# Optimization experiments

Hardware: AMD Instinct MI355X
Metric: run time of the kernel (lower is better)

## Reference

```python
import jax, jax.numpy as jnp
import numpy as np

N = 131072
MUL = 32

# e3nn normalization (irrep_normalization='component', path_normalization='element'):
# alpha_path = w3j_norm * sqrt(ir_out.dim / sum_{paths into same i_out} mul1*mul2)
# 0e output: paths (0e,0e)->0e and (1o,1o)->0e -> fan = 2*32*32 = 2048
# 1o output: paths (0e,1o)->1o and (1o,0e)->1o -> fan = 2048
# 1e output: path  (1o,1o)->1e               -> fan = 1024
_A000 = 1.0 / np.sqrt(2048.0)                    # w3j(0,0,0)=1,        sqrt(1/2048)
_A011 = (1.0 / np.sqrt(3.0)) * np.sqrt(3.0 / 2048.0)   # = 1/sqrt(2048)
_A101 = _A011
_A110 = (1.0 / np.sqrt(3.0)) * np.sqrt(1.0 / 2048.0)
_A111 = (1.0 / np.sqrt(6.0)) * np.sqrt(3.0 / 1024.0)   # = 1/sqrt(2048)


def setup_inputs() -> dict:
    key = jax.random.key(0)
    ks = jax.random.split(key, 7)
    return {
        "x1": jax.random.normal(ks[0], (N, 4 * MUL), dtype=jnp.float32),
        "x2": jax.random.normal(ks[1], (N, 4 * MUL), dtype=jnp.float32),
        "w000": jax.random.normal(ks[2], (MUL, MUL, MUL), dtype=jnp.float32),
        "w011": jax.random.normal(ks[3], (MUL, MUL, MUL), dtype=jnp.float32),
        "w101": jax.random.normal(ks[4], (MUL, MUL, MUL), dtype=jnp.float32),
        "w110": jax.random.normal(ks[5], (MUL, MUL, MUL), dtype=jnp.float32),
        "w111": jax.random.normal(ks[6], (MUL, MUL, MUL), dtype=jnp.float32),
    }


def _uvw(a, b, w):
    # scalar-channel path: out_zw = sum_uv a_zu b_zv w_uvw
    return jnp.einsum('zu,zv,uvw->zw', a, b, w, optimize=True)


def _tp(x1, x2, w000, w011, w101, w110, w111):
    n = x1.shape[0]
    x1s = x1[:, :MUL]                       # [z,u]    0e
    x1v = x1[:, MUL:].reshape(n, MUL, 3)    # [z,u,3]  1o
    x2s = x2[:, :MUL]
    x2v = x2[:, MUL:].reshape(n, MUL, 3)

    # (0e,0e)->0e and (1o,1o)->0e  (w3j(1,1,0) = delta_ij/sqrt(3), folded into alpha)
    p000 = _uvw(x1s, x2s, w000)                                  # [z,w]
    p110 = jnp.einsum('zui,zvi,uvw->zw', x1v, x2v, w110, optimize=True)
    out0 = _A000 * p000 + _A110 * p110                           # [z,w]

    # (0e,1o)->1o and (1o,0e)->1o  (w3j(0,1,1) = delta/sqrt(3), folded into alpha)
    p011 = jnp.einsum('zu,zvj,uvw->zwj', x1s, x2v, w011, optimize=True)
    p101 = jnp.einsum('zui,zv,uvw->zwi', x1v, x2s, w101, optimize=True)
    out1 = _A011 * p011 + _A101 * p101                           # [z,w,3]

    # (1o,1o)->1e via levi-civita (w3j(1,1,1) = eps/sqrt(6), folded into alpha)
    # out_zwk = sum_ij eps_ijk * uvw-contraction; expand cross product per component
    comps = []
    for (i, j) in ((1, 2), (2, 0), (0, 1)):
        comps.append(_uvw(x1v[:, :, i], x2v[:, :, j], w111)
                     - _uvw(x1v[:, :, j], x2v[:, :, i], w111))
    out2 = _A111 * jnp.stack(comps, axis=-1)                     # [z,w,3]

    return jnp.concatenate(
        [out0, out1.reshape(n, -1), out2.reshape(n, -1)], axis=-1)  # [z,224]


def reference(x1, x2, w000, w011, w101, w110, w111):
    return _tp(x1, x2, w000, w011, w101, w110, w111)
```

## Files before the change

### kernel.cpp

```cpp
#include <hip/hip_runtime.h>


typedef _Float16 f16;
typedef f16 f16x8 __attribute__((ext_vector_type(8)));
typedef float f32x4 __attribute__((ext_vector_type(4)));

#define MFMA16(a, b, c) __builtin_amdgcn_mfma_f32_16x16x32_f16(a, b, c, 0, 0, 0)

#define SC_COMMON 0.022097086912079608f
#define SC_110    0.012757759118834242f

__global__ void prep_w(const float* __restrict__ w000, const float* __restrict__ w011,
                       const float* __restrict__ w101, const float* __restrict__ w110,
                       const float* __restrict__ w111, f16* __restrict__ wsW)
{
    int flat = blockIdx.x * 256 + threadIdx.x;
    if (flat >= 5 * 32768) return;
    int c = flat >> 15;
    int r = flat & 32767;
    int j    = r & 7;
    int lane = (r >> 3) & 63;
    int half = (r >> 9) & 1;
    int u    = r >> 10;
    int n = lane & 15, q = lane >> 4;
    int v = q * 8 + j;
    int w = n + 16 * half;
    const float* src; float sc;
    switch (c) {
        case 0: src = w000; sc = SC_COMMON; break;
        case 1: src = w110; sc = SC_110;    break;
        case 2: src = w011; sc = SC_COMMON; break;
        case 3: src = w101; sc = SC_COMMON; break;
        default: src = w111; sc = SC_COMMON; break;
    }
    wsW[flat] = (f16)(sc * src[u * 1024 + v * 32 + w]);
}


template <int A>
__device__ __forceinline__ f16x8 load_group(const float* __restrict__ x1row, int u0)
{
    f16x8 g;
    if (A == 0) {
#pragma unroll
        for (int j = 0; j < 8; ++j) g[j] = (f16)x1row[u0 + j];
    } else {
#pragma unroll
        for (int j = 0; j < 8; ++j) g[j] = (f16)x1row[32 + 3 * (u0 + j) + (A - 1)];
    }
    return g;
}

template <int MODE, int P, int Q>
__device__ __forceinline__ void gemm_half(f32x4 (&acc)[2][2],
                                          const f16* __restrict__ ldsW,
                                          const f16* __restrict__ ldsX2,
                                          const float* __restrict__ x1blk,
                                          int waveRow, int lane, int u0base)
{
    const int m = lane & 15, qd = lane >> 4;

    f16x8 f2a[2], f2b[2], f2c[2];
#pragma unroll
    for (int s = 0; s < 2; ++s) {
        const f16* base = ldsX2 + (waveRow + s * 16 + m) * 128 + qd * 8;
        if (MODE == 0) {
            f2a[s] = *(const f16x8*)(base + Q * 32);
        } else if (MODE == 1) {
            f2a[s] = *(const f16x8*)(base + 1 * 32);
            f2b[s] = *(const f16x8*)(base + 2 * 32);
            f2c[s] = *(const f16x8*)(base + 3 * 32);
        } else {
            f2a[s] = *(const f16x8*)(base + Q * 32);
            f2b[s] = *(const f16x8*)(base + P * 32);
        }
    }

    const float* x1row[2];
#pragma unroll
    for (int s = 0; s < 2; ++s)
        x1row[s] = x1blk + (size_t)(waveRow + s * 16 + m) * 128;

#pragma unroll
    for (int ug = 0; ug < 2; ++ug) {
        const int u0 = u0base + ug * 8;
        f16x8 g1[2], g2[2], g3[2];
#pragma unroll
        for (int s = 0; s < 2; ++s) {
            if (MODE == 0) {
                g1[s] = load_group<P>(x1row[s], u0);
            } else if (MODE == 1) {
                g1[s] = load_group<1>(x1row[s], u0);
                g2[s] = load_group<2>(x1row[s], u0);
                g3[s] = load_group<3>(x1row[s], u0);
            } else {
                g1[s] = load_group<P>(x1row[s], u0);
                g2[s] = load_group<Q>(x1row[s], u0);
            }
        }
#pragma unroll
        for (int uu = 0; uu < 8; ++uu) {
            const int ul = (u0base + ug * 8 + uu) - u0base + (u0base ? 0 : 0);
            const int ulocal = ug * 8 + uu;
            (void)ul;
            f16x8 a[2];
#pragma unroll
            for (int s = 0; s < 2; ++s) {
                if (MODE == 0) {
                    a[s] = g1[s][uu] * f2a[s];
                } else if (MODE == 1) {
                    a[s] = g1[s][uu] * f2a[s] + g2[s][uu] * f2b[s] + g3[s][uu] * f2c[s];
                } else {
                    a[s] = g1[s][uu] * f2a[s] - g2[s][uu] * f2b[s];
                }
            }
#pragma unroll
            for (int half = 0; half < 2; ++half) {
                f16x8 b = *(const f16x8*)(ldsW + ((ulocal * 2 + half) * 64 + lane) * 8);
#pragma unroll
                for (int s = 0; s < 2; ++s)
                    acc[s][half] = MFMA16(a[s], b, acc[s][half]);
            }
        }
    }
}

__device__ __forceinline__ void stage_w(f16* __restrict__ ldsW,
                                        const f16* __restrict__ src, int tid)
{
#pragma unroll
    for (int it = 0; it < 8; ++it) {
        int o = it * 2048 + tid * 8;
        *(f16x8*)(ldsW + o) = *(const f16x8*)(src + o);
    }
}

__global__ __launch_bounds__(256, 2)
void tp_main(const float* __restrict__ x1, const float* __restrict__ x2,
             const f16* __restrict__ wsW, float* __restrict__ out)
{
    __shared__ __align__(16) f16 ldsW[16384];
    __shared__ __align__(16) f16 ldsX2[16384];

    const int tid = threadIdx.x;
    const int lane = tid & 63;
    const int wv = tid >> 6;
    const int waveRow = wv * 32;

    const float* x1blk = x1 + (size_t)blockIdx.x * 128 * 128;
    const float* x2blk = x2 + (size_t)blockIdx.x * 128 * 128;

#pragma unroll
    for (int it = 0; it < 16; ++it) {
        int idx4 = it * 256 + tid;
        float4 val = ((const float4*)x2blk)[idx4];
        float vv[4] = {val.x, val.y, val.z, val.w};
        int flat = idx4 * 4;
        int row = flat >> 7, col = flat & 127;
#pragma unroll
        for (int e = 0; e < 4; ++e) {
            int cc = col + e;
            int arr, ii;
            if (cc < 32) { arr = 0; ii = cc; }
            else { int c2 = cc - 32; arr = 1 + (c2 % 3); ii = c2 / 3; }
            ldsX2[row * 128 + arr * 32 + ii] = (f16)vv[e];
        }
    }

    const int m = lane & 15, qd = lane >> 4;
    const int rowb = blockIdx.x * 128 + waveRow + qd * 4;

    {
        f32x4 acc[2][2] = {};
        for (int c = 0; c < 2; ++c)
            for (int h = 0; h < 2; ++h) {
                __syncthreads();
                stage_w(ldsW, wsW + c * 32768 + h * 16384, tid);
                __syncthreads();
                if (c == 0) gemm_half<0, 0, 0>(acc, ldsW, ldsX2, x1blk, waveRow, lane, h * 16);
                else        gemm_half<1, 0, 0>(acc, ldsW, ldsX2, x1blk, waveRow, lane, h * 16);
            }
#pragma unroll
        for (int s = 0; s < 2; ++s)
#pragma unroll
            for (int half = 0; half < 2; ++half)
#pragma unroll
                for (int r = 0; r < 4; ++r) {
                    int z = rowb + s * 16 + r;
                    out[(size_t)z * 224 + half * 16 + m] = acc[s][half][r];
                }
    }

    {
        f32x4 acc[3][2][2] = {};
        for (int h = 0; h < 2; ++h) {
            __syncthreads();
            stage_w(ldsW, wsW + 2 * 32768 + h * 16384, tid);
            __syncthreads();
            gemm_half<0, 0, 1>(acc[0], ldsW, ldsX2, x1blk, waveRow, lane, h * 16);
            gemm_half<0, 0, 2>(acc[1], ldsW, ldsX2, x1blk, waveRow, lane, h * 16);
            gemm_half<0, 0, 3>(acc[2], ldsW, ldsX2, x1blk, waveRow, lane, h * 16);
        }
        for (int h = 0; h < 2; ++h) {
            __syncthreads();
            stage_w(ldsW, wsW + 3 * 32768 + h * 16384, tid);
            __syncthreads();
            gemm_half<0, 1, 0>(acc[0], ldsW, ldsX2, x1blk, waveRow, lane, h * 16);
            gemm_half<0, 2, 0>(acc[1], ldsW, ldsX2, x1blk, waveRow, lane, h * 16);
            gemm_half<0, 3, 0>(acc[2], ldsW, ldsX2, x1blk, waveRow, lane, h * 16);
        }
#pragma unroll
        for (int s = 0; s < 2; ++s)
#pragma unroll
            for (int half = 0; half < 2; ++half)
#pragma unroll
                for (int r = 0; r < 4; ++r) {
                    int z = rowb + s * 16 + r;
                    int wcol = half * 16 + m;
                    size_t base = (size_t)z * 224 + 32 + 3 * wcol;
                    out[base + 0] = acc[0][s][half][r];
                    out[base + 1] = acc[1][s][half][r];
                    out[base + 2] = acc[2][s][half][r];
                }
    }

    {
        f32x4 acc[3][2][2] = {};
        for (int h = 0; h < 2; ++h) {
            __syncthreads();
            stage_w(ldsW, wsW + 4 * 32768 + h * 16384, tid);
            __syncthreads();
            gemm_half<2, 2, 3>(acc[0], ldsW, ldsX2, x1blk, waveRow, lane, h * 16);
            gemm_half<2, 3, 1>(acc[1], ldsW, ldsX2, x1blk, waveRow, lane, h * 16);
            gemm_half<2, 1, 2>(acc[2], ldsW, ldsX2, x1blk, waveRow, lane, h * 16);
        }
#pragma unroll
        for (int s = 0; s < 2; ++s)
#pragma unroll
            for (int half = 0; half < 2; ++half)
#pragma unroll
                for (int r = 0; r < 4; ++r) {
                    int z = rowb + s * 16 + r;
                    int wcol = half * 16 + m;
                    size_t base = (size_t)z * 224 + 128 + 3 * wcol;
                    out[base + 0] = acc[0][s][half][r];
                    out[base + 1] = acc[1][s][half][r];
                    out[base + 2] = acc[2][s][half][r];
                }
    }
}

extern "C" void kernel_launch(void* const* d_in, const int* in_sizes, int n_in,
                              void* d_out, int out_size, void* d_ws, size_t ws_size,
                              hipStream_t stream)
{
    const float* x1   = (const float*)d_in[0];
    const float* x2   = (const float*)d_in[1];
    const float* w000 = (const float*)d_in[2];
    const float* w011 = (const float*)d_in[3];
    const float* w101 = (const float*)d_in[4];
    const float* w110 = (const float*)d_in[5];
    const float* w111 = (const float*)d_in[6];
    float* out = (float*)d_out;
    f16* wsW = (f16*)d_ws;

    hipLaunchKernelGGL(prep_w, dim3(640), dim3(256), 0, stream,
                       w000, w011, w101, w110, w111, wsW);

    int n = in_sizes[0] / 128;
    hipLaunchKernelGGL(tp_main, dim3(n / 128), dim3(256), 0, stream,
                       x1, x2, wsW, out);
}
```

Measured before the change: 345.6 us.

## Switch to 32x32x16 MFMA with register-resident x1/x2 fragments and async LDS weight staging

Replaces the 16x16x32 MFMA tiling with 32x32x16 MFMA so each wave computes a 32-row by 32-column tile per instruction. The weight layout in prep_w is reordered to match. x1 and x2 rows are now loaded once per thread into f16 register fragments instead of staging x2 through LDS and re-reading x1 from global memory in every GEMM pass. Weight staging now uses global_load_lds direct-to-LDS copies. This removes repeated global loads of x1 and the x2 LDS transpose, at the cost of much higher register pressure from holding all fragments and 16-wide accumulators.

```diff
diff --git a/kernel.cpp b/kernel.cpp
--- a/kernel.cpp
+++ b/kernel.cpp
@@ -3,9 +3,9 @@
 
 typedef _Float16 f16;
 typedef f16 f16x8 __attribute__((ext_vector_type(8)));
-typedef float f32x4 __attribute__((ext_vector_type(4)));
-
-#define MFMA16(a, b, c) __builtin_amdgcn_mfma_f32_16x16x32_f16(a, b, c, 0, 0, 0)
+typedef float f32x16 __attribute__((ext_vector_type(16)));
+
+#define MFMA32(a, b, c) __builtin_amdgcn_mfma_f32_32x32x16_f16(a, b, c, 0, 0, 0)
 
 #define SC_COMMON 0.022097086912079608f
 #define SC_110    0.012757759118834242f
@@ -16,15 +16,14 @@
 {
     int flat = blockIdx.x * 256 + threadIdx.x;
     if (flat >= 5 * 32768) return;
-    int c = flat >> 15;
-    int r = flat & 32767;
+    int c    = flat >> 15;
+    int r    = flat & 32767;
     int j    = r & 7;
     int lane = (r >> 3) & 63;
-    int half = (r >> 9) & 1;
+    int vh   = (r >> 9) & 1;
     int u    = r >> 10;
-    int n = lane & 15, q = lane >> 4;
-    int v = q * 8 + j;
-    int w = n + 16 * half;
+    int v = vh * 16 + ((lane >> 5) << 3) + j;
+    int w = lane & 31;
     const float* src; float sc;
     switch (c) {
         case 0: src = w000; sc = SC_COMMON; break;
@@ -36,102 +35,49 @@
     wsW[flat] = (f16)(sc * src[u * 1024 + v * 32 + w]);
 }
 
-
-template <int A>
-__device__ __forceinline__ f16x8 load_group(const float* __restrict__ x1row, int u0)
-{
-    f16x8 g;
-    if (A == 0) {
-#pragma unroll
-        for (int j = 0; j < 8; ++j) g[j] = (f16)x1row[u0 + j];
-    } else {
-#pragma unroll
-        for (int j = 0; j < 8; ++j) g[j] = (f16)x1row[32 + 3 * (u0 + j) + (A - 1)];
-    }
-    return g;
-}
-
-template <int MODE, int P, int Q>
-__device__ __forceinline__ void gemm_half(f32x4 (&acc)[2][2],
-                                          const f16* __restrict__ ldsW,
-                                          const f16* __restrict__ ldsX2,
-                                          const float* __restrict__ x1blk,
-                                          int waveRow, int lane, int u0base)
-{
-    const int m = lane & 15, qd = lane >> 4;
-
-    f16x8 f2a[2], f2b[2], f2c[2];
-#pragma unroll
-    for (int s = 0; s < 2; ++s) {
-        const f16* base = ldsX2 + (waveRow + s * 16 + m) * 128 + qd * 8;
-        if (MODE == 0) {
-            f2a[s] = *(const f16x8*)(base + Q * 32);
-        } else if (MODE == 1) {
-            f2a[s] = *(const f16x8*)(base + 1 * 32);
-            f2b[s] = *(const f16x8*)(base + 2 * 32);
-            f2c[s] = *(const f16x8*)(base + 3 * 32);
-        } else {
-            f2a[s] = *(const f16x8*)(base + Q * 32);
-            f2b[s] = *(const f16x8*)(base + P * 32);
-        }
-    }
-
-    const float* x1row[2];
-#pragma unroll
-    for (int s = 0; s < 2; ++s)
-        x1row[s] = x1blk + (size_t)(waveRow + s * 16 + m) * 128;
-
-#pragma unroll
-    for (int ug = 0; ug < 2; ++ug) {
-        const int u0 = u0base + ug * 8;
-        f16x8 g1[2], g2[2], g3[2];
-#pragma unroll
-        for (int s = 0; s < 2; ++s) {
+template <int U0, int MODE, int NA>
+__device__ __forceinline__ void do_stage(f32x16 (&acc)[NA],
+                                         const f16* __restrict__ ldsW,
+                                         const f16x8 (&f1g)[4][4],
+                                         const f16x8 (&f2g)[4][2], int lane)
+{
+#pragma unroll
+    for (int ul = 0; ul < 16; ++ul) {
+        const int u = U0 + ul;
+#pragma unroll
+        for (int vh = 0; vh < 2; ++vh) {
+            f16x8 b = *(const f16x8*)(ldsW + ul * 1024 + vh * 512 + lane * 8);
             if (MODE == 0) {
-                g1[s] = load_group<P>(x1row[s], u0);
+                f16x8 a = f1g[0][u >> 3][u & 7] * f2g[0][vh];
+                acc[0] = MFMA32(a, b, acc[0]);
             } else if (MODE == 1) {
-                g1[s] = load_group<1>(x1row[s], u0);
-                g2[s] = load_group<2>(x1row[s], u0);
-                g3[s] = load_group<3>(x1row[s], u0);
+                f16x8 a = f1g[1][u >> 3][u & 7] * f2g[1][vh];
+                a += f1g[2][u >> 3][u & 7] * f2g[2][vh];
+                a += f1g[3][u >> 3][u & 7] * f2g[3][vh];
+                acc[0] = MFMA32(a, b, acc[0]);
+            } else if (MODE == 2) {
+#pragma unroll
+                for (int j = 0; j < 3; ++j) {
+                    f16x8 a = f1g[0][u >> 3][u & 7] * f2g[1 + j][vh];
+                    acc[j] = MFMA32(a, b, acc[j]);
+                }
+            } else if (MODE == 3) {
+#pragma unroll
+                for (int j = 0; j < 3; ++j) {
+                    f16x8 a = f1g[1 + j][u >> 3][u & 7] * f2g[0][vh];
+                    acc[j] = MFMA32(a, b, acc[j]);
+                }
             } else {
-                g1[s] = load_group<P>(x1row[s], u0);
-                g2[s] = load_group<Q>(x1row[s], u0);
-            }
-        }
-#pragma unroll
-        for (int uu = 0; uu < 8; ++uu) {
-            const int ul = (u0base + ug * 8 + uu) - u0base + (u0base ? 0 : 0);
-            const int ulocal = ug * 8 + uu;
-            (void)ul;
-            f16x8 a[2];
-#pragma unroll
-            for (int s = 0; s < 2; ++s) {
-                if (MODE == 0) {
-                    a[s] = g1[s][uu] * f2a[s];
-                } else if (MODE == 1) {
-                    a[s] = g1[s][uu] * f2a[s] + g2[s][uu] * f2b[s] + g3[s][uu] * f2c[s];
-                } else {
-                    a[s] = g1[s][uu] * f2a[s] - g2[s][uu] * f2b[s];
+#pragma unroll
+                for (int k = 0; k < 3; ++k) {
+                    const int P = (k == 0) ? 2 : (k == 1) ? 3 : 1;
+                    const int Q = (k == 0) ? 3 : (k == 1) ? 1 : 2;
+                    f16x8 a = f1g[P][u >> 3][u & 7] * f2g[Q][vh]
+                            - f1g[Q][u >> 3][u & 7] * f2g[P][vh];
+                    acc[k] = MFMA32(a, b, acc[k]);
                 }
             }
-#pragma unroll
-            for (int half = 0; half < 2; ++half) {
-                f16x8 b = *(const f16x8*)(ldsW + ((ulocal * 2 + half) * 64 + lane) * 8);
-#pragma unroll
-                for (int s = 0; s < 2; ++s)
-                    acc[s][half] = MFMA16(a[s], b, acc[s][half]);
-            }
-        }
-    }
-}
-
-__device__ __forceinline__ void stage_w(f16* __restrict__ ldsW,
-                                        const f16* __restrict__ src, int tid)
-{
-#pragma unroll
-    for (int it = 0; it < 8; ++it) {
-        int o = it * 2048 + tid * 8;
-        *(f16x8*)(ldsW + o) = *(const f16x8*)(src + o);
+        }
     }
 }
 
@@ -140,113 +86,114 @@
              const f16* __restrict__ wsW, float* __restrict__ out)
 {
     __shared__ __align__(16) f16 ldsW[16384];
-    __shared__ __align__(16) f16 ldsX2[16384];
-
-    const int tid = threadIdx.x;
-    const int lane = tid & 63;
-    const int wv = tid >> 6;
-    const int waveRow = wv * 32;
-
-    const float* x1blk = x1 + (size_t)blockIdx.x * 128 * 128;
-    const float* x2blk = x2 + (size_t)blockIdx.x * 128 * 128;
-
-#pragma unroll
-    for (int it = 0; it < 16; ++it) {
-        int idx4 = it * 256 + tid;
-        float4 val = ((const float4*)x2blk)[idx4];
-        float vv[4] = {val.x, val.y, val.z, val.w};
-        int flat = idx4 * 4;
-        int row = flat >> 7, col = flat & 127;
-#pragma unroll
-        for (int e = 0; e < 4; ++e) {
-            int cc = col + e;
-            int arr, ii;
-            if (cc < 32) { arr = 0; ii = cc; }
-            else { int c2 = cc - 32; arr = 1 + (c2 % 3); ii = c2 / 3; }
-            ldsX2[row * 128 + arr * 32 + ii] = (f16)vv[e];
-        }
-    }
-
-    const int m = lane & 15, qd = lane >> 4;
-    const int rowb = blockIdx.x * 128 + waveRow + qd * 4;
-
-    {
-        f32x4 acc[2][2] = {};
-        for (int c = 0; c < 2; ++c)
-            for (int h = 0; h < 2; ++h) {
-                __syncthreads();
-                stage_w(ldsW, wsW + c * 32768 + h * 16384, tid);
-                __syncthreads();
-                if (c == 0) gemm_half<0, 0, 0>(acc, ldsW, ldsX2, x1blk, waveRow, lane, h * 16);
-                else        gemm_half<1, 0, 0>(acc, ldsW, ldsX2, x1blk, waveRow, lane, h * 16);
-            }
-#pragma unroll
-        for (int s = 0; s < 2; ++s)
-#pragma unroll
-            for (int half = 0; half < 2; ++half)
-#pragma unroll
-                for (int r = 0; r < 4; ++r) {
-                    int z = rowb + s * 16 + r;
-                    out[(size_t)z * 224 + half * 16 + m] = acc[s][half][r];
-                }
-    }
-
-    {
-        f32x4 acc[3][2][2] = {};
-        for (int h = 0; h < 2; ++h) {
-            __syncthreads();
-            stage_w(ldsW, wsW + 2 * 32768 + h * 16384, tid);
-            __syncthreads();
-            gemm_half<0, 0, 1>(acc[0], ldsW, ldsX2, x1blk, waveRow, lane, h * 16);
-            gemm_half<0, 0, 2>(acc[1], ldsW, ldsX2, x1blk, waveRow, lane, h * 16);
-            gemm_half<0, 0, 3>(acc[2], ldsW, ldsX2, x1blk, waveRow, lane, h * 16);
-        }
-        for (int h = 0; h < 2; ++h) {
-            __syncthreads();
-            stage_w(ldsW, wsW + 3 * 32768 + h * 16384, tid);
-            __syncthreads();
-            gemm_half<0, 1, 0>(acc[0], ldsW, ldsX2, x1blk, waveRow, lane, h * 16);
-            gemm_half<0, 2, 0>(acc[1], ldsW, ldsX2, x1blk, waveRow, lane, h * 16);
-            gemm_half<0, 3, 0>(acc[2], ldsW, ldsX2, x1blk, waveRow, lane, h * 16);
-        }
-#pragma unroll
-        for (int s = 0; s < 2; ++s)
-#pragma unroll
-            for (int half = 0; half < 2; ++half)
-#pragma unroll
-                for (int r = 0; r < 4; ++r) {
-                    int z = rowb + s * 16 + r;
-                    int wcol = half * 16 + m;
-                    size_t base = (size_t)z * 224 + 32 + 3 * wcol;
-                    out[base + 0] = acc[0][s][half][r];
-                    out[base + 1] = acc[1][s][half][r];
-                    out[base + 2] = acc[2][s][half][r];
-                }
-    }
-
-    {
-        f32x4 acc[3][2][2] = {};
-        for (int h = 0; h < 2; ++h) {
-            __syncthreads();
-            stage_w(ldsW, wsW + 4 * 32768 + h * 16384, tid);
-            __syncthreads();
-            gemm_half<2, 2, 3>(acc[0], ldsW, ldsX2, x1blk, waveRow, lane, h * 16);
-            gemm_half<2, 3, 1>(acc[1], ldsW, ldsX2, x1blk, waveRow, lane, h * 16);
-            gemm_half<2, 1, 2>(acc[2], ldsW, ldsX2, x1blk, waveRow, lane, h * 16);
-        }
-#pragma unroll
-        for (int s = 0; s < 2; ++s)
-#pragma unroll
-            for (int half = 0; half < 2; ++half)
-#pragma unroll
-                for (int r = 0; r < 4; ++r) {
-                    int z = rowb + s * 16 + r;
-                    int wcol = half * 16 + m;
-                    size_t base = (size_t)z * 224 + 128 + 3 * wcol;
-                    out[base + 0] = acc[0][s][half][r];
-                    out[base + 1] = acc[1][s][half][r];
-                    out[base + 2] = acc[2][s][half][r];
-                }
+
+    const int tid = threadIdx.x, lane = tid & 63, wv = tid >> 6;
+    const int rowBase = blockIdx.x * 128 + wv * 32;
+    const int mrow = lane & 31;
+    const int half = lane >> 5;
+    const int klo = half * 8;
+    const float4* x1r4 = (const float4*)(x1 + (size_t)(rowBase + mrow) * 128);
+    const float4* x2r4 = (const float4*)(x2 + (size_t)(rowBase + mrow) * 128);
+
+    f16x8 f1g[4][4];
+    {
+        float b0[32];
+#pragma unroll
+        for (int g = 0; g < 8; ++g) ((float4*)b0)[g] = x1r4[g];
+#pragma unroll
+        for (int g = 0; g < 4; ++g)
+#pragma unroll
+            for (int j = 0; j < 8; ++j) f1g[0][g][j] = (f16)b0[g * 8 + j];
+        float b1[96];
+#pragma unroll
+        for (int g = 0; g < 24; ++g) ((float4*)b1)[g] = x1r4[8 + g];
+#pragma unroll
+        for (int i = 0; i < 3; ++i)
+#pragma unroll
+            for (int g = 0; g < 4; ++g)
+#pragma unroll
+                for (int j = 0; j < 8; ++j)
+                    f1g[1 + i][g][j] = (f16)b1[3 * (g * 8 + j) + i];
+    }
+
+    f16x8 f2g[4][2];
+    {
+        float c0[16];
+#pragma unroll
+        for (int g = 0; g < 2; ++g) ((float4*)c0)[g]     = x2r4[klo / 4 + g];
+#pragma unroll
+        for (int g = 0; g < 2; ++g) ((float4*)c0)[2 + g] = x2r4[4 + klo / 4 + g];
+#pragma unroll
+        for (int vh = 0; vh < 2; ++vh)
+#pragma unroll
+            for (int j = 0; j < 8; ++j) f2g[0][vh][j] = (f16)c0[vh * 8 + j];
+        float c1[48];
+        const int base1 = (32 + 3 * klo) / 4;
+#pragma unroll
+        for (int g = 0; g < 6; ++g) ((float4*)c1)[g]     = x2r4[base1 + g];
+#pragma unroll
+        for (int g = 0; g < 6; ++g) ((float4*)c1)[6 + g] = x2r4[base1 + 12 + g];
+#pragma unroll
+        for (int i = 0; i < 3; ++i)
+#pragma unroll
+            for (int vh = 0; vh < 2; ++vh)
+#pragma unroll
+                for (int j = 0; j < 8; ++j)
+                    f2g[1 + i][vh][j] = (f16)c1[vh * 24 + 3 * j + i];
+    }
+
+    auto stage = [&](int c, int h) {
+        __syncthreads();
+        const f16* src = wsW + c * 32768 + h * 16384;
+#pragma unroll
+        for (int it = 0; it < 8; ++it) {
+            int o = (it * 256 + tid) * 8;
+            __builtin_amdgcn_global_load_lds(
+                (const __attribute__((address_space(1))) void*)(src + o),
+                (__attribute__((address_space(3))) void*)(ldsW + o), 16, 0, 0);
+        }
+        __syncthreads();
+    };
+
+    {
+        f32x16 acc[1] = {};
+        stage(0, 0); do_stage<0, 0>(acc, ldsW, f1g, f2g, lane);
+        stage(0, 1); do_stage<16, 0>(acc, ldsW, f1g, f2g, lane);
+        stage(1, 0); do_stage<0, 1>(acc, ldsW, f1g, f2g, lane);
+        stage(1, 1); do_stage<16, 1>(acc, ldsW, f1g, f2g, lane);
+#pragma unroll
+        for (int reg = 0; reg < 16; ++reg) {
+            int r = (reg & 3) + 8 * (reg >> 2) + 4 * half;
+            out[(size_t)(rowBase + r) * 224 + mrow] = acc[0][reg];
+        }
+    }
+    {
+        f32x16 acc[3] = {};
+        stage(2, 0); do_stage<0, 2>(acc, ldsW, f1g, f2g, lane);
+        stage(2, 1); do_stage<16, 2>(acc, ldsW, f1g, f2g, lane);
+        stage(3, 0); do_stage<0, 3>(acc, ldsW, f1g, f2g, lane);
+        stage(3, 1); do_stage<16, 3>(acc, ldsW, f1g, f2g, lane);
+#pragma unroll
+        for (int reg = 0; reg < 16; ++reg) {
+            int r = (reg & 3) + 8 * (reg >> 2) + 4 * half;
+            size_t base = (size_t)(rowBase + r) * 224 + 32 + 3 * mrow;
+            out[base + 0] = acc[0][reg];
+            out[base + 1] = acc[1][reg];
+            out[base + 2] = acc[2][reg];
+        }
+    }
+    {
+        f32x16 acc[3] = {};
+        stage(4, 0); do_stage<0, 4>(acc, ldsW, f1g, f2g, lane);
+        stage(4, 1); do_stage<16, 4>(acc, ldsW, f1g, f2g, lane);
+#pragma unroll
+        for (int reg = 0; reg < 16; ++reg) {
+            int r = (reg & 3) + 8 * (reg >> 2) + 4 * half;
+            size_t base = (size_t)(rowBase + r) * 224 + 128 + 3 * mrow;
+            out[base + 0] = acc[0][reg];
+            out[base + 1] = acc[1][reg];
+            out[base + 2] = acc[2][reg];
+        }
     }
 }
 
```

Result: faster. 292.3 us (-15.4%).
